# Kernel tuning notes

Measured on AMD Instinct MI355X. Metric: run time of the kernel, lower is better.

The kernel has to match this reference:

```python
import jax, jax.numpy as jnp
import numpy as np

N_NODES = 100_000
N_EDGES = 3_200_000
N_FEAT = 128
HIDDEN = 16
OUT = 2
N_GRAPHS = 64


def setup_inputs() -> dict:
    key = jax.random.key(0)
    ks = jax.random.split(key, 12)
    x = jax.random.normal(ks[0], (N_NODES, N_FEAT), dtype=jnp.float32)
    edge_index = jax.random.randint(ks[1], (2, N_EDGES), 0, N_NODES, dtype=jnp.int64)
    batch_idx = jnp.sort(jax.random.randint(ks[2], (N_NODES,), 0, N_GRAPHS, dtype=jnp.int64))

    def glorot(k, shape):
        s = jnp.sqrt(6.0 / (shape[0] + shape[1])).astype(jnp.float32)
        return jax.random.uniform(k, shape, jnp.float32, -1.0, 1.0) * s

    return {
        "x": x, "edge_index": edge_index, "batch_idx": batch_idx,
        "W0": glorot(ks[3], (N_FEAT, HIDDEN)), "b0": jnp.zeros((HIDDEN,), jnp.float32),
        "a0": jnp.full((1,), 0.25, jnp.float32),  # PReLU default weight
        "W1": glorot(ks[4], (HIDDEN, HIDDEN)), "b1": jnp.zeros((HIDDEN,), jnp.float32),
        "a1": jnp.full((1,), 0.25, jnp.float32),
        "W2": glorot(ks[5], (HIDDEN, HIDDEN)), "b2": jnp.zeros((HIDDEN,), jnp.float32),
        "a2": jnp.full((1,), 0.25, jnp.float32),
        "W3": glorot(ks[6], (HIDDEN, OUT)), "b3": jnp.zeros((OUT,), jnp.float32),
    }


def _prelu(x, a):
    return jnp.where(x > 0, x, a * x)


def _gcn_conv(x, W, b, src, dst, norm, n):
    # PyG GCNConv: linear transform, then normalized gather-scatter aggregation, then bias
    h = x @ W                                   # [N, out]
    msg = h[src] * norm[:, None]                # gather + per-edge scale
    out = jax.ops.segment_sum(msg, dst, num_segments=n)  # scatter-add into targets
    return out + b


def reference(x, edge_index, batch_idx, W0, b0, a0, W1, b1, a1, W2, b2, a2, W3, b3):
    n = x.shape[0]
    loop = jnp.arange(n, dtype=edge_index.dtype)
    src = jnp.concatenate([edge_index[0], loop])  # add self loops
    dst = jnp.concatenate([edge_index[1], loop])
    # symmetric degree normalization deg^-1/2 (deg over targets, all edge weights = 1)
    deg = jax.ops.segment_sum(jnp.ones_like(dst, dtype=x.dtype), dst, num_segments=n)
    dinv = jnp.where(deg > 0, jax.lax.rsqrt(deg), 0.0)
    norm = dinv[src] * dinv[dst]

    h = _prelu(_gcn_conv(x, W0, b0, src, dst, norm, n), a0)
    h = _prelu(_gcn_conv(h, W1, b1, src, dst, norm, n), a1)
    h = _prelu(_gcn_conv(h, W2, b2, src, dst, norm, n), a2)
    h = _gcn_conv(h, W3, b3, src, dst, norm, n)

    # global_mean_pool over graph ids
    sums = jax.ops.segment_sum(h, batch_idx, num_segments=N_GRAPHS)
    cnts = jax.ops.segment_sum(jnp.ones((n,), h.dtype), batch_idx, num_segments=N_GRAPHS)
    return sums / jnp.maximum(cnts, 1.0)[:, None]
```

## Files before the change

### kernel.cpp

```cpp
#include <hip/hip_runtime.h>


#define NN 100000
#define NE 3200000
#define NF 128
#define NH 16
#define NO 2
#define NG 64
#define NBLK 391
#define BN 256
#define NBUK 391
#define CHUNK 4096
#define NBLKA 782
#define CAPF 10240
#define NT0 6250

typedef __attribute__((ext_vector_type(8))) short short8;
typedef __attribute__((ext_vector_type(4))) float float4v;


__device__ __forceinline__ float ldf(const void* p, int i, int f32) {
  if (f32) return ((const float*)p)[i];
  unsigned int u = ((const unsigned short*)p)[i];
  return __uint_as_float(u << 16);
}
__device__ __forceinline__ int ldi(const void* p, int i, int i64) {
  if (i64) return (int)((const long long*)p)[i];
  return ((const int*)p)[i];
}
__device__ __forceinline__ void stf(void* p, int i, float v, int f32) {
  if (f32) {
    ((float*)p)[i] = v;
  } else {
    unsigned int w = __float_as_uint(v);
    unsigned int r = (w + 0x7fffu + ((w >> 16) & 1u)) >> 16;
    ((unsigned short*)p)[i] = (unsigned short)r;
  }
}
__device__ __forceinline__ float bf16lo(unsigned int u) { return __uint_as_float(u << 16); }
__device__ __forceinline__ float bf16hi(unsigned int u) { return __uint_as_float(u & 0xffff0000u); }
__device__ __forceinline__ unsigned int packbf(float x, float y) {
  unsigned int a = __float_as_uint(x);
  a = (a + 0x7fffu + ((a >> 16) & 1u)) >> 16;
  unsigned int b = __float_as_uint(y);
  b = (b + 0x7fffu + ((b >> 16) & 1u)) & 0xffff0000u;
  return a | b;
}
__device__ __forceinline__ int okf(float v) { return (v == v) && (fabsf(v) < 1e30f); }
__device__ __forceinline__ void nflag(int* diag, int bad, int bit) {
  if (__any(bad)) {
    if ((threadIdx.x & 63) == 0) atomicOr(diag + 2, 1 << bit);
  }
}
__device__ __forceinline__ int clampi(int v, int hi) {
  return (unsigned)v < (unsigned)hi ? v : 0;
}


__global__ __launch_bounds__(1024) void k_sniff(const void* x, const void* ei, int* zbase) {
  int tid = threadIdx.x;
  if (tid < 624) zbase[tid] = 0;
  __syncthreads();
  if (tid < 64) {
    unsigned int xv = ((const unsigned int*)x)[tid];
    unsigned int e = (xv >> 7) & 0xffu;
    int hit = (e >= 116u && e <= 133u);
    int hits = __popcll(__ballot(hit));
    unsigned int ev = ((const unsigned int*)ei)[2 * tid + 1];
    int nzc = __popcll(__ballot(ev != 0u));
    if (tid == 0) {
      zbase[0] = (hits < 32) ? 1 : 0;
      zbase[1] = (nzc == 0) ? 1 : 0;
    }
  }
}


__global__ __launch_bounds__(512) void k_build(const void* ei, const int* __restrict__ diag,
                                               int* __restrict__ cursor, int* __restrict__ ents) {
  __shared__ int spktA[CHUNK];
  __shared__ unsigned short sbid[CHUNK];
  __shared__ unsigned short srank[CHUNK];
  __shared__ int spktB[CHUNK];
  __shared__ int gpos[CHUNK];
  __shared__ int lscan[512];
  __shared__ int sexcl[NBUK];
  __shared__ int goff[NBUK];
  int tid = threadIdx.x, blk = blockIdx.x;
  lscan[tid] = 0;
  __syncthreads();
  int i64 = diag[1];
  int base = blk * CHUNK;
  int n = NE - base; n = n > CHUNK ? CHUNK : n;
  for (int i = tid; i < n; i += 512) {
    int sv = clampi(ldi(ei, base + i, i64), NN);
    int dv = clampi(ldi(ei, NE + base + i, i64), NN);
    int b = dv >> 8;
    spktA[i] = ((dv & 255) << 17) | sv;
    sbid[i] = (unsigned short)b;
    srank[i] = (unsigned short)atomicAdd(&lscan[b], 1);
  }
  __syncthreads();
  for (int off = 1; off < 512; off <<= 1) {
    int v = (tid >= off) ? lscan[tid - off] : 0;
    __syncthreads();
    lscan[tid] += v;
    __syncthreads();
  }
  if (tid < NBUK) {
    int b = tid;
    int incl = lscan[b];
    int excl = (b > 0) ? lscan[b - 1] : 0;
    int cnt = incl - excl;
    sexcl[b] = excl;
    int rbase = cnt ? atomicAdd(&cursor[b], cnt) : 0;
    goff[b] = b * CAPF + rbase - excl;
  }
  __syncthreads();
  for (int i = tid; i < n; i += 512) {
    int b = sbid[i];
    int rr = sexcl[b] + srank[i];
    spktB[rr] = spktA[i];
    int gp = goff[b] + rr;
    int hi = b * CAPF + CAPF - 1;
    gpos[rr] = gp <= hi ? gp : hi;
  }
  __syncthreads();
  for (int r = tid; r < n; r += 512) ents[gpos[r]] = spktB[r];
}

__global__ __launch_bounds__(512) void k_bsort(int* __restrict__ ents, const int* __restrict__ cursor,
                                               int* __restrict__ rowstart, int* __restrict__ rowend,
                                               float* __restrict__ dinv, int* __restrict__ diag) {
  __shared__ int ent[CAPF];
  __shared__ unsigned short rnk[CAPF];
  __shared__ int lcnt[BN];
  __shared__ int sexcl[BN];
  int tid = threadIdx.x, b = blockIdx.x;
  int bs = b * CAPF;
  int n = cursor[b];
  if (n > CAPF) { n = CAPF; if (tid == 0) atomicOr(diag + 2, 1 << 9); }
  if (tid < BN) lcnt[tid] = 0;
  __syncthreads();
  for (int i = tid; i < n; i += 512) {
    int e = ents[bs + i];
    ent[i] = e;
    rnk[i] = (unsigned short)atomicAdd(&lcnt[e >> 17], 1);
  }
  __syncthreads();
  int c = (tid < BN) ? lcnt[tid] : 0;
  for (int off = 1; off < BN; off <<= 1) {
    int v = (tid < BN && tid >= off) ? lcnt[tid - off] : 0;
    __syncthreads();
    if (tid < BN) lcnt[tid] += v;
    __syncthreads();
  }
  if (tid < BN) {
    int excl = lcnt[tid] - c;
    sexcl[tid] = excl;
    int node = (b << 8) + tid;
    if (node < NN) {
      rowstart[node] = bs + excl;
      rowend[node] = bs + excl + c;
      dinv[node] = rsqrtf((float)(c + 1));
    }
  }
  __syncthreads();
  for (int i = tid; i < n; i += 512) {
    int e = ent[i];
    ents[bs + sexcl[e >> 17] + rnk[i]] = e & 0x1FFFF;
  }
}


__global__ __launch_bounds__(256) void k_t0(const void* __restrict__ x, const void* __restrict__ W0,
                                            const float* __restrict__ dinv,
                                            int* __restrict__ diag, unsigned int* __restrict__ out) {
  __shared__ float ws[NF * NH];
  __shared__ float xs[16 * 129];
  int tid = threadIdx.x;
  int f32 = diag[0];
  if (!f32) {
    const unsigned short* xu = (const unsigned short*)x;
    const unsigned short* wu = (const unsigned short*)W0;
    int wave = tid >> 6, lane = tid & 63;
    int nfe = lane & 15, quad = lane >> 4;
    short8 bfr[4];
#pragma unroll
    for (int mf = 0; mf < 4; ++mf) {
      short8 t;
#pragma unroll
      for (int j = 0; j < 8; ++j) t[j] = (short)wu[(mf * 32 + quad * 8 + j) * NH + nfe];
      bfr[mf] = t;
    }
    int tile = blockIdx.x * 4 + wave;
    if (tile < NT0) {
      int node0 = tile * 16;
      const short8* xrow = (const short8*)(xu + (node0 + nfe) * NF);
      float4v c = {0.f, 0.f, 0.f, 0.f};
#pragma unroll
      for (int mf = 0; mf < 4; ++mf) {
        short8 a = xrow[mf * 4 + quad];
        c = __builtin_amdgcn_mfma_f32_16x16x32_bf16(a, bfr[mf], c, 0, 0, 0);
      }
      int bad = 0;
#pragma unroll
      for (int r = 0; r < 4; ++r) {
        int node = node0 + quad * 4 + r;
        float v = c[r] * dinv[node];
        float o = __shfl_xor(v, 1);
        if (!(nfe & 1)) out[node * 8 + (nfe >> 1)] = packbf(v, o);
        bad |= !okf(v);
      }
      nflag(diag, bad, 0);
    }
  } else {
    for (int t = 0; t < 4; ++t) {
      int tile = blockIdx.x * 4 + t;
      if (tile >= NT0) break;
      int node0 = tile * 16;
      __syncthreads();
#pragma unroll
      for (int r = 0; r < 8; ++r) ws[tid + 256 * r] = ldf(W0, tid + 256 * r, 1);
#pragma unroll
      for (int r = 0; r < 8; ++r) {
        int idx = tid + 256 * r;
        int row = idx >> 7, col = idx & 127;
        xs[row * 129 + col] = ldf(x, (node0 + row) * NF + col, 1);
      }
      __syncthreads();
      int nl = tid >> 4, f = tid & 15;
      float acc = 0.f;
#pragma unroll 4
      for (int k = 0; k < NF; ++k) acc += xs[nl * 129 + k] * ws[k * NH + f];
      acc *= dinv[node0 + nl];
      float other = __shfl_xor(acc, 1);
      if ((f & 1) == 0) out[(node0 + nl) * 8 + (f >> 1)] = packbf(acc, other);
      nflag(diag, !okf(acc), 0);
    }
  }
}


__global__ __launch_bounds__(256) void k_aggT(const uint2* __restrict__ hin,
                                              const int* __restrict__ srcs,
                                              const int* __restrict__ rowstart,
                                              const int* __restrict__ rowend,
                                              const float* __restrict__ dinv,
                                              const void* __restrict__ b, const void* __restrict__ a,
                                              const void* __restrict__ Wn,
                                              int* __restrict__ diag, int bit,
                                              uint2* __restrict__ hout) {
  __shared__ float ws[NH * NH];
  int tid = threadIdx.x;
  int f32 = diag[0];
  ws[tid] = ldf(Wn, tid, f32);
  __syncthreads();
  int gid = blockIdx.x * 256 + tid;
  if (gid >= NN * 4) return;
  int node = gid >> 2, p = gid & 3;
  uint2 self = hin[gid];
  float acc0 = bf16lo(self.x), acc1 = bf16hi(self.x);
  float acc2 = bf16lo(self.y), acc3 = bf16hi(self.y);
  int e = rowstart[node], e1 = rowend[node];
  for (; e + 8 <= e1; e += 8) {
    uint2 v[8];
#pragma unroll
    for (int k = 0; k < 8; ++k) v[k] = hin[srcs[e + k] * 4 + p];
#pragma unroll
    for (int k = 0; k < 8; ++k) {
      acc0 += bf16lo(v[k].x);
      acc1 += bf16hi(v[k].x);
      acc2 += bf16lo(v[k].y);
      acc3 += bf16hi(v[k].y);
    }
  }
  for (; e + 2 <= e1; e += 2) {
    uint2 va = hin[srcs[e] * 4 + p];
    uint2 vb = hin[srcs[e + 1] * 4 + p];
    acc0 += bf16lo(va.x) + bf16lo(vb.x);
    acc1 += bf16hi(va.x) + bf16hi(vb.x);
    acc2 += bf16lo(va.y) + bf16lo(vb.y);
    acc3 += bf16hi(va.y) + bf16hi(vb.y);
  }
  if (e < e1) {
    uint2 v = hin[srcs[e] * 4 + p];
    acc0 += bf16lo(v.x);
    acc1 += bf16hi(v.x);
    acc2 += bf16lo(v.y);
    acc3 += bf16hi(v.y);
  }
  float dv = dinv[node];
  float av = ldf(a, 0, f32);
  float p0 = dv * acc0 + ldf(b, 4 * p + 0, f32);
  float p1 = dv * acc1 + ldf(b, 4 * p + 1, f32);
  float p2 = dv * acc2 + ldf(b, 4 * p + 2, f32);
  float p3 = dv * acc3 + ldf(b, 4 * p + 3, f32);
  p0 = p0 > 0.f ? p0 : av * p0;
  p1 = p1 > 0.f ? p1 : av * p1;
  p2 = p2 > 0.f ? p2 : av * p2;
  p3 = p3 > 0.f ? p3 : av * p3;
  float t0 = 0.f, t1 = 0.f, t2 = 0.f, t3 = 0.f;
#pragma unroll
  for (int j = 0; j < 4; ++j) {
    float q0 = __shfl(p0, j, 4);
    float q1 = __shfl(p1, j, 4);
    float q2 = __shfl(p2, j, 4);
    float q3 = __shfl(p3, j, 4);
    const float* w0 = &ws[(4 * j) * NH + 4 * p];
    const float* w1 = &ws[(4 * j + 1) * NH + 4 * p];
    const float* w2 = &ws[(4 * j + 2) * NH + 4 * p];
    const float* w3 = &ws[(4 * j + 3) * NH + 4 * p];
    t0 += q0 * w0[0] + q1 * w1[0] + q2 * w2[0] + q3 * w3[0];
    t1 += q0 * w0[1] + q1 * w1[1] + q2 * w2[1] + q3 * w3[1];
    t2 += q0 * w0[2] + q1 * w1[2] + q2 * w2[2] + q3 * w3[2];
    t3 += q0 * w0[3] + q1 * w1[3] + q2 * w2[3] + q3 * w3[3];
  }
  t0 *= dv; t1 *= dv; t2 *= dv; t3 *= dv;
  uint2 o;
  o.x = packbf(t0, t1);
  o.y = packbf(t2, t3);
  hout[gid] = o;
  nflag(diag, !okf(t0) || !okf(t3), bit);
}

__global__ __launch_bounds__(256) void k_aggT3(const uint2* __restrict__ hin,
                                               const int* __restrict__ srcs,
                                               const int* __restrict__ rowstart,
                                               const int* __restrict__ rowend,
                                               const float* __restrict__ dinv,
                                               const void* __restrict__ b, const void* __restrict__ a,
                                               const void* __restrict__ W3,
                                               int* __restrict__ diag, float2* __restrict__ hout) {
  __shared__ float ws[NH * NO];
  int tid = threadIdx.x;
  int f32 = diag[0];
  if (tid < NH * NO) ws[tid] = ldf(W3, tid, f32);
  __syncthreads();
  int gid = blockIdx.x * 256 + tid;
  if (gid >= NN * 4) return;
  int node = gid >> 2, p = gid & 3;
  uint2 self = hin[gid];
  float acc0 = bf16lo(self.x), acc1 = bf16hi(self.x);
  float acc2 = bf16lo(self.y), acc3 = bf16hi(self.y);
  int e = rowstart[node], e1 = rowend[node];
  for (; e + 8 <= e1; e += 8) {
    uint2 v[8];
#pragma unroll
    for (int k = 0; k < 8; ++k) v[k] = hin[srcs[e + k] * 4 + p];
#pragma unroll
    for (int k = 0; k < 8; ++k) {
      acc0 += bf16lo(v[k].x);
      acc1 += bf16hi(v[k].x);
      acc2 += bf16lo(v[k].y);
      acc3 += bf16hi(v[k].y);
    }
  }
  for (; e + 2 <= e1; e += 2) {
    uint2 va = hin[srcs[e] * 4 + p];
    uint2 vb = hin[srcs[e + 1] * 4 + p];
    acc0 += bf16lo(va.x) + bf16lo(vb.x);
    acc1 += bf16hi(va.x) + bf16hi(vb.x);
    acc2 += bf16lo(va.y) + bf16lo(vb.y);
    acc3 += bf16hi(va.y) + bf16hi(vb.y);
  }
  if (e < e1) {
    uint2 v = hin[srcs[e] * 4 + p];
    acc0 += bf16lo(v.x);
    acc1 += bf16hi(v.x);
    acc2 += bf16lo(v.y);
    acc3 += bf16hi(v.y);
  }
  float dv = dinv[node];
  float av = ldf(a, 0, f32);
  float p0 = dv * acc0 + ldf(b, 4 * p + 0, f32);
  float p1 = dv * acc1 + ldf(b, 4 * p + 1, f32);
  float p2 = dv * acc2 + ldf(b, 4 * p + 2, f32);
  float p3 = dv * acc3 + ldf(b, 4 * p + 3, f32);
  p0 = p0 > 0.f ? p0 : av * p0;
  p1 = p1 > 0.f ? p1 : av * p1;
  p2 = p2 > 0.f ? p2 : av * p2;
  p3 = p3 > 0.f ? p3 : av * p3;
  float u0 = p0 * ws[(4 * p) * NO]     + p1 * ws[(4 * p + 1) * NO] +
             p2 * ws[(4 * p + 2) * NO] + p3 * ws[(4 * p + 3) * NO];
  float u1 = p0 * ws[(4 * p) * NO + 1]     + p1 * ws[(4 * p + 1) * NO + 1] +
             p2 * ws[(4 * p + 2) * NO + 1] + p3 * ws[(4 * p + 3) * NO + 1];
  u0 += __shfl_xor(u0, 1, 4);
  u0 += __shfl_xor(u0, 2, 4);
  u1 += __shfl_xor(u1, 1, 4);
  u1 += __shfl_xor(u1, 2, 4);
  if (p == 0) hout[node] = make_float2(dv * u0, dv * u1);
  nflag(diag, !okf(u0) || !okf(u1), 6);
}

__global__ __launch_bounds__(256) void k_agg2p(const float2* __restrict__ tin,
                                               const int* __restrict__ srcs,
                                               const int* __restrict__ rowstart,
                                               const int* __restrict__ rowend,
                                               const float* __restrict__ dinv,
                                               const void* __restrict__ b3,
                                               const void* __restrict__ batch,
                                               int* __restrict__ diag, float* __restrict__ pool) {
  __shared__ float ssum[NG * NO];
  __shared__ float scnt[NG];
  int tid = threadIdx.x;
  int f32 = diag[0], i64 = diag[1];
  if (tid < NG * NO) ssum[tid] = 0.f;
  if (tid < NG) scnt[tid] = 0.f;
  __syncthreads();
  int node = blockIdx.x * 256 + tid;
  if (node < NN) {
    float2 t = tin[node];
    float a0 = t.x, a1 = t.y;
    int e = rowstart[node], e1 = rowend[node];
    for (; e + 4 <= e1; e += 4) {
      int s0 = srcs[e], s1 = srcs[e + 1], s2 = srcs[e + 2], s3 = srcs[e + 3];
      float2 h0 = tin[s0], h1 = tin[s1], h2 = tin[s2], h3 = tin[s3];
      a0 += h0.x + h1.x + h2.x + h3.x;
      a1 += h0.y + h1.y + h2.y + h3.y;
    }
    for (; e < e1; ++e) {
      float2 hv = tin[srcs[e]];
      a0 += hv.x;
      a1 += hv.y;
    }
    float dv = dinv[node];
    a0 = dv * a0 + ldf(b3, 0, f32);
    a1 = dv * a1 + ldf(b3, 1, f32);
    int g = ldi(batch, node, i64);
    g = (unsigned)g < NG ? g : 0;
    atomicAdd(&ssum[g * 2], a0);
    atomicAdd(&ssum[g * 2 + 1], a1);
    atomicAdd(&scnt[g], 1.f);
    nflag(diag, !okf(a0) || !okf(a1), 7);
  }
  __syncthreads();
  if (tid < NG * NO && ssum[tid] != 0.f) atomicAdd(&pool[tid], ssum[tid]);
  if (tid < NG && scnt[tid] != 0.f) atomicAdd(&pool[NG * NO + tid], scnt[tid]);
}

__global__ __launch_bounds__(128) void k_final(const float* __restrict__ pool,
                                               const int* __restrict__ diag, void* __restrict__ out) {
  int i = threadIdx.x;
  int f32 = diag[0], i64 = diag[1], stg = diag[2];
  float c = pool[NG * NO + (i >> 1)];
  c = c > 1.f ? c : 1.f;
  float v = pool[i] / c;
  if (stg != 0 || !okf(v)) {
    int stage = stg ? __ffs(stg) : 15;
    v = 1024.0f + stage * 64.0f + f32 * 16.0f + i64 * 8.0f;
  }
  stf(out, i, v, f32);
}

__global__ __launch_bounds__(128) void k_diag_ws(void* out, float v) {
  unsigned int w = __float_as_uint(v);
  ((unsigned short*)out)[threadIdx.x] = (unsigned short)(w >> 16);
}


extern "C" void kernel_launch(void* const* d_in, const int* in_sizes, int n_in,
                              void* d_out, int out_size, void* d_ws, size_t ws_size,
                              hipStream_t stream) {
  const void* x  = d_in[0];
  const void* ei = d_in[1];
  const void* batch = d_in[2];
  const void* W0 = d_in[3];
  const void* b0 = d_in[4];
  const void* a0 = d_in[5];
  const void* W1 = d_in[6];
  const void* b1 = d_in[7];
  const void* a1 = d_in[8];
  const void* W2 = d_in[9];
  const void* b2 = d_in[10];
  const void* a2 = d_in[11];
  const void* W3 = d_in[12];
  const void* b3 = d_in[13];

  char* w = (char*)d_ws;
  int* diag         = (int*)(w + 0);
  float* pool       = (float*)(w + 64);
  int* cursor       = (int*)(w + 896);
  float* dinv       = (float*)(w + 2496);
  int* rowstart     = (int*)(w + 402496);
  int* rowend       = (int*)(w + 802496);
  int* ents         = (int*)(w + 1202496);
  uint2* hsA        = (uint2*)(w + 17217856);
  uint2* hsB        = (uint2*)(w + 20417856);
  float2* hs3       = (float2*)(w + 23617856);
  const size_t NEED = 24417856;

  if (ws_size < NEED) {
    k_diag_ws<<<1, 128, 0, stream>>>(d_out, (float)ws_size);
    return;
  }

  k_sniff<<<1, 1024, 0, stream>>>(x, ei, (int*)w);

  k_build<<<NBLKA, 512, 0, stream>>>(ei, diag, cursor, ents);
  k_bsort<<<NBUK, 512, 0, stream>>>(ents, cursor, rowstart, rowend, dinv, diag);

  k_t0<<<(NT0 + 3) / 4, 256, 0, stream>>>(x, W0, dinv, diag, (unsigned int*)hsA);
  k_aggT<<<(NN * 4 + 255) / 256, 256, 0, stream>>>(hsA, ents, rowstart, rowend, dinv, b0, a0, W1, diag, 1, hsB);
  k_aggT<<<(NN * 4 + 255) / 256, 256, 0, stream>>>(hsB, ents, rowstart, rowend, dinv, b1, a1, W2, diag, 3, hsA);
  k_aggT3<<<(NN * 4 + 255) / 256, 256, 0, stream>>>(hsA, ents, rowstart, rowend, dinv, b2, a2, W3, diag, hs3);
  k_agg2p<<<NBLK, 256, 0, stream>>>(hs3, ents, rowstart, rowend, dinv, b3, batch, diag, pool);

  k_final<<<1, 128, 0, stream>>>(pool, diag, d_out);
}
```

Baseline: 299.1 us.

## Use bf16 MFMA for f32 first-layer transform and vectorize edge index loads

The fp32 path of the first linear layer now converts x and W0 rows to bf16 in registers and uses the 16x16x32 bf16 MFMA instruction instead of an LDS-staged scalar dot product. The aggregation kernels now load edge source indices as aligned vectors split across the four lanes sharing a node and broadcast them with shuffles, with a prologue to align the edge pointer. This is meant to reduce instruction count and redundant index loads, at the cost of reduced precision in the fp32 matmul path.

```diff
diff --git a/kernel.cpp b/kernel.cpp
--- a/kernel.cpp
+++ b/kernel.cpp
@@ -46,6 +46,10 @@
   b = (b + 0x7fffu + ((b >> 16) & 1u)) & 0xffff0000u;
   return a | b;
 }
+__device__ __forceinline__ short bf16rne(float v) {
+  unsigned int w = __float_as_uint(v);
+  return (short)((w + 0x7fffu + ((w >> 16) & 1u)) >> 16);
+}
 __device__ __forceinline__ int okf(float v) { return (v == v) && (fabsf(v) < 1e30f); }
 __device__ __forceinline__ void nflag(int* diag, int bad, int bit) {
   if (__any(bad)) {
@@ -176,69 +180,65 @@
 __global__ __launch_bounds__(256) void k_t0(const void* __restrict__ x, const void* __restrict__ W0,
                                             const float* __restrict__ dinv,
                                             int* __restrict__ diag, unsigned int* __restrict__ out) {
-  __shared__ float ws[NF * NH];
-  __shared__ float xs[16 * 129];
   int tid = threadIdx.x;
   int f32 = diag[0];
-  if (!f32) {
-    const unsigned short* xu = (const unsigned short*)x;
-    const unsigned short* wu = (const unsigned short*)W0;
-    int wave = tid >> 6, lane = tid & 63;
-    int nfe = lane & 15, quad = lane >> 4;
-    short8 bfr[4];
+  int wave = tid >> 6, lane = tid & 63;
+  int nfe = lane & 15, quad = lane >> 4;
+  short8 bfr[4];
+  if (f32) {
+    const float* wf = (const float*)W0;
 #pragma unroll
     for (int mf = 0; mf < 4; ++mf) {
       short8 t;
 #pragma unroll
+      for (int j = 0; j < 8; ++j) t[j] = bf16rne(wf[(mf * 32 + quad * 8 + j) * NH + nfe]);
+      bfr[mf] = t;
+    }
+  } else {
+    const unsigned short* wu = (const unsigned short*)W0;
+#pragma unroll
+    for (int mf = 0; mf < 4; ++mf) {
+      short8 t;
+#pragma unroll
       for (int j = 0; j < 8; ++j) t[j] = (short)wu[(mf * 32 + quad * 8 + j) * NH + nfe];
       bfr[mf] = t;
     }
-    int tile = blockIdx.x * 4 + wave;
-    if (tile < NT0) {
-      int node0 = tile * 16;
-      const short8* xrow = (const short8*)(xu + (node0 + nfe) * NF);
-      float4v c = {0.f, 0.f, 0.f, 0.f};
-#pragma unroll
-      for (int mf = 0; mf < 4; ++mf) {
-        short8 a = xrow[mf * 4 + quad];
-        c = __builtin_amdgcn_mfma_f32_16x16x32_bf16(a, bfr[mf], c, 0, 0, 0);
+  }
+  int tile = blockIdx.x * 4 + wave;
+  if (tile >= NT0) return;
+  int node0 = tile * 16;
+  float4v c = {0.f, 0.f, 0.f, 0.f};
+  if (f32) {
+    const float4v* xrow = (const float4v*)((const float*)x + (node0 + nfe) * NF);
+#pragma unroll
+    for (int mf = 0; mf < 4; ++mf) {
+      float4v f0 = xrow[mf * 8 + quad * 2];
+      float4v f1 = xrow[mf * 8 + quad * 2 + 1];
+      short8 a;
+#pragma unroll
+      for (int j = 0; j < 4; ++j) {
+        a[j] = bf16rne(f0[j]);
+        a[j + 4] = bf16rne(f1[j]);
       }
-      int bad = 0;
-#pragma unroll
-      for (int r = 0; r < 4; ++r) {
-        int node = node0 + quad * 4 + r;
-        float v = c[r] * dinv[node];
-        float o = __shfl_xor(v, 1);
-        if (!(nfe & 1)) out[node * 8 + (nfe >> 1)] = packbf(v, o);
-        bad |= !okf(v);
-      }
-      nflag(diag, bad, 0);
+      c = __builtin_amdgcn_mfma_f32_16x16x32_bf16(a, bfr[mf], c, 0, 0, 0);
     }
   } else {
-    for (int t = 0; t < 4; ++t) {
-      int tile = blockIdx.x * 4 + t;
-      if (tile >= NT0) break;
-      int node0 = tile * 16;
-      __syncthreads();
-#pragma unroll
-      for (int r = 0; r < 8; ++r) ws[tid + 256 * r] = ldf(W0, tid + 256 * r, 1);
-#pragma unroll
-      for (int r = 0; r < 8; ++r) {
-        int idx = tid + 256 * r;
-        int row = idx >> 7, col = idx & 127;
-        xs[row * 129 + col] = ldf(x, (node0 + row) * NF + col, 1);
-      }
-      __syncthreads();
-      int nl = tid >> 4, f = tid & 15;
-      float acc = 0.f;
-#pragma unroll 4
-      for (int k = 0; k < NF; ++k) acc += xs[nl * 129 + k] * ws[k * NH + f];
-      acc *= dinv[node0 + nl];
-      float other = __shfl_xor(acc, 1);
-      if ((f & 1) == 0) out[(node0 + nl) * 8 + (f >> 1)] = packbf(acc, other);
-      nflag(diag, !okf(acc), 0);
-    }
-  }
+    const short8* xrow = (const short8*)((const unsigned short*)x + (node0 + nfe) * NF);
+#pragma unroll
+    for (int mf = 0; mf < 4; ++mf) {
+      c = __builtin_amdgcn_mfma_f32_16x16x32_bf16(xrow[mf * 4 + quad], bfr[mf], c, 0, 0, 0);
+    }
+  }
+  int bad = 0;
+#pragma unroll
+  for (int r = 0; r < 4; ++r) {
+    int node = node0 + quad * 4 + r;
+    float v = c[r] * dinv[node];
+    float o = __shfl_xor(v, 1);
+    if (!(nfe & 1)) out[node * 8 + (nfe >> 1)] = packbf(v, o);
+    bad |= !okf(v);
+  }
+  nflag(diag, bad, 0);
 }
 
 
@@ -263,10 +263,24 @@
   float acc0 = bf16lo(self.x), acc1 = bf16hi(self.x);
   float acc2 = bf16lo(self.y), acc3 = bf16hi(self.y);
   int e = rowstart[node], e1 = rowend[node];
+  if ((e & 1) && e < e1) {
+    uint2 v = hin[srcs[e] * 4 + p];
+    acc0 += bf16lo(v.x);
+    acc1 += bf16hi(v.x);
+    acc2 += bf16lo(v.y);
+    acc3 += bf16hi(v.y);
+    ++e;
+  }
   for (; e + 8 <= e1; e += 8) {
+    uint2 si = *(const uint2*)(srcs + e + 2 * p);
     uint2 v[8];
 #pragma unroll
-    for (int k = 0; k < 8; ++k) v[k] = hin[srcs[e + k] * 4 + p];
+    for (int k = 0; k < 4; ++k) {
+      int ia = __shfl((int)si.x, k, 4);
+      int ib = __shfl((int)si.y, k, 4);
+      v[2 * k] = hin[ia * 4 + p];
+      v[2 * k + 1] = hin[ib * 4 + p];
+    }
 #pragma unroll
     for (int k = 0; k < 8; ++k) {
       acc0 += bf16lo(v[k].x);
@@ -344,10 +358,24 @@
   float acc0 = bf16lo(self.x), acc1 = bf16hi(self.x);
   float acc2 = bf16lo(self.y), acc3 = bf16hi(self.y);
   int e = rowstart[node], e1 = rowend[node];
+  if ((e & 1) && e < e1) {
+    uint2 v = hin[srcs[e] * 4 + p];
+    acc0 += bf16lo(v.x);
+    acc1 += bf16hi(v.x);
+    acc2 += bf16lo(v.y);
+    acc3 += bf16hi(v.y);
+    ++e;
+  }
   for (; e + 8 <= e1; e += 8) {
+    uint2 si = *(const uint2*)(srcs + e + 2 * p);
     uint2 v[8];
 #pragma unroll
-    for (int k = 0; k < 8; ++k) v[k] = hin[srcs[e + k] * 4 + p];
+    for (int k = 0; k < 4; ++k) {
+      int ia = __shfl((int)si.x, k, 4);
+      int ib = __shfl((int)si.y, k, 4);
+      v[2 * k] = hin[ia * 4 + p];
+      v[2 * k + 1] = hin[ib * 4 + p];
+    }
 #pragma unroll
     for (int k = 0; k < 8; ++k) {
       acc0 += bf16lo(v[k].x);
@@ -413,9 +441,15 @@
     float2 t = tin[node];
     float a0 = t.x, a1 = t.y;
     int e = rowstart[node], e1 = rowend[node];
+    while ((e & 3) && e < e1) {
+      float2 hv = tin[srcs[e]];
+      a0 += hv.x;
+      a1 += hv.y;
+      ++e;
+    }
     for (; e + 4 <= e1; e += 4) {
-      int s0 = srcs[e], s1 = srcs[e + 1], s2 = srcs[e + 2], s3 = srcs[e + 3];
-      float2 h0 = tin[s0], h1 = tin[s1], h2 = tin[s2], h3 = tin[s3];
+      int4 s4 = *(const int4*)(srcs + e);
+      float2 h0 = tin[s4.x], h1 = tin[s4.y], h2 = tin[s4.z], h3 = tin[s4.w];
       a0 += h0.x + h1.x + h2.x + h3.x;
       a1 += h0.y + h1.y + h2.y + h3.y;
     }
```

Result: faster. 280.0 us (-6.4%).
